# Kernel optimization log

Hardware: AMD Instinct MI355X
Metric: run time of the kernel (lower is better)

## Reference

```python
import jax, jax.numpy as jnp
import numpy as np
from jax import lax

NSAMPLE = 16
NEG_SLOPE = 0.1


def leaky(x):
    return jnp.where(x >= 0, x, NEG_SLOPE * x)


def setup_inputs() -> dict:
    key = jax.random.key(0)
    ks = jax.random.split(key, 8)
    B, N1, N2, D = 4, 4096, 4096, 64
    C_in, C_mid, C_out = D + D + 3, 128, 128  # 131 -> 128 -> 128
    xyz1 = jax.random.normal(ks[0], (B, 3, N1), jnp.float32)
    xyz2 = jax.random.normal(ks[1], (B, 3, N2), jnp.float32)
    points1 = jax.random.normal(ks[2], (B, D, N1), jnp.float32)
    points2 = jax.random.normal(ks[3], (B, D, N2), jnp.float32)
    W1 = jax.random.normal(ks[4], (C_mid, C_in), jnp.float32) * 0.05
    b1 = jnp.zeros((C_mid,), jnp.float32)
    W2 = jax.random.normal(ks[5], (C_out, C_mid), jnp.float32) * 0.05
    b2 = jnp.zeros((C_out,), jnp.float32)
    return {"xyz1": xyz1, "xyz2": xyz2, "points1": points1, "points2": points2,
            "W1": W1, "b1": b1, "W2": W2, "b2": b2}


def reference(xyz1, xyz2, points1, points2, W1, b1, W2, b2):
    B, _, N1 = xyz1.shape
    x1 = jnp.transpose(xyz1, (0, 2, 1))      # [B,N1,3]
    x2 = jnp.transpose(xyz2, (0, 2, 1))      # [B,N2,3]
    p1 = jnp.transpose(points1, (0, 2, 1))   # [B,N1,D1]
    p2 = jnp.transpose(points2, (0, 2, 1))   # [B,N2,D2]

    # knn_point: k smallest squared distances from each x1 point into x2
    d2 = (jnp.sum(x1 * x1, -1)[:, :, None]
          + jnp.sum(x2 * x2, -1)[:, None, :]
          - 2.0 * jnp.einsum('bnc,bmc->bnm', x1, x2))  # [B,N1,N2]
    _, knn_idx = lax.top_k(-d2, NSAMPLE)     # [B,N1,K]

    bidx = jnp.arange(B)[:, None, None]
    neighbor_xyz = x2[bidx, knn_idx]         # [B,N1,K,3]
    direction_xyz = neighbor_xyz - x1[:, :, None, :]
    gp2 = p2[bidx, knn_idx]                  # [B,N1,K,D2]
    gp1 = jnp.broadcast_to(p1[:, :, None, :], (B, N1, NSAMPLE, p1.shape[-1]))
    feat = jnp.concatenate([gp1, gp2, direction_xyz], axis=-1)  # [B,N1,K,131]

    h = leaky(jnp.einsum('oc,bnkc->bnko', W1, feat) + b1)
    h = leaky(jnp.einsum('oc,bnkc->bnko', W2, h) + b2)           # [B,N1,K,C_out]

    dist = jnp.maximum(jnp.linalg.norm(direction_xyz, axis=3), 1e-10)  # [B,N1,K]
    inv = 1.0 / dist
    weights = inv / jnp.sum(inv, axis=2, keepdims=True)          # [B,N1,K]

    cost = jnp.einsum('bnk,bnko->bon', weights, h)               # [B,C_out,N1]
    return cost
```

## Files before the change

### kernel.cpp

```cpp
#include <hip/hip_runtime.h>

typedef unsigned short u16;
typedef unsigned int u32;
typedef unsigned long long u64;
typedef __bf16 bf16x8 __attribute__((ext_vector_type(8)));
typedef float f32x4 __attribute__((ext_vector_type(4)));

#define MFMA16(a, b, c) __builtin_amdgcn_mfma_f32_16x16x32_bf16(a, b, c, 0, 0, 0)

static __device__ __forceinline__ u16 f2bf(float f) {
  union { float f; u32 u; } v; v.f = f;
  u32 u = v.u;
  u32 r = (u + 0x7FFFu + ((u >> 16) & 1u)) >> 16;
  return (u16)r;
}

static __device__ __forceinline__ bf16x8 ld16(const u16* p) {
  return __builtin_bit_cast(bf16x8, *(const uint4*)p);
}

static __device__ __forceinline__ u64 u64min(u64 a, u64 b) { return a < b ? a : b; }

static __device__ __forceinline__ u64 bitonic64(u64 v, int lane) {
#pragma unroll
  for (int k = 2; k <= 64; k <<= 1) {
#pragma unroll
    for (int j = k >> 1; j > 0; j >>= 1) {
      u64 o = __shfl_xor(v, j, 64);
      bool up = ((lane & k) == 0);
      bool lower = ((lane & j) == 0);
      u64 mn = v < o ? v : o;
      u64 mx = v < o ? o : v;
      v = (lower == up) ? mn : mx;
    }
  }
  return v;
}

static __device__ __forceinline__ void bitonic64_2(u64& a, u64& b, int lane) {
#pragma unroll
  for (int k = 2; k <= 64; k <<= 1) {
#pragma unroll
    for (int j = k >> 1; j > 0; j >>= 1) {
      u64 oa = __shfl_xor(a, j, 64);
      u64 ob = __shfl_xor(b, j, 64);
      bool up = ((lane & k) == 0);
      bool lower = ((lane & j) == 0);
      bool sel = (lower == up);
      u64 mna = a < oa ? a : oa, mxa = a < oa ? oa : a;
      u64 mnb = b < ob ? b : ob, mxb = b < ob ? ob : b;
      a = sel ? mna : mxa;
      b = sel ? mnb : mxb;
    }
  }
}

static __device__ __forceinline__ void bitonic32_2(u64& a, u64& b, int lane) {
#pragma unroll
  for (int k = 2; k <= 32; k <<= 1) {
#pragma unroll
    for (int j = k >> 1; j > 0; j >>= 1) {
      u64 oa = __shfl_xor(a, j, 64);
      u64 ob = __shfl_xor(b, j, 64);
      bool up = ((lane & k) == 0);
      bool lower = ((lane & j) == 0);
      bool sel = (lower == up);
      u64 mna = a < oa ? a : oa, mxa = a < oa ? oa : a;
      u64 mnb = b < ob ? b : ob, mxb = b < ob ? ob : b;
      a = sel ? mna : mxa;
      b = sel ? mnb : mxb;
    }
  }
}

static __device__ __forceinline__ u32 fkey(float f) {
  u32 bb = __float_as_uint(f);
  u32 sgn = (u32)((int)bb >> 31);
  return bb ^ (sgn | 0x80000000u);
}

static __device__ __forceinline__ float ikey(u32 k) {
  u32 bb = (k & 0x80000000u) ? (k ^ 0x80000000u) : ~k;
  return __uint_as_float(bb);
}

static __device__ __forceinline__ float d2of(float x, float y, float z, float s1,
                                             f32x4 c) {
  float dt = __builtin_fmaf(z, c[2], __builtin_fmaf(y, c[1], __fmul_rn(x, c[0])));
  return __fsub_rn(__fadd_rn(s1, c[3]), __fmul_rn(2.0f, dt));
}

__global__ __launch_bounds__(1024, 2) void knn_prep(
    const float* __restrict__ xyz1, const float* __restrict__ xyz2,
    const float* __restrict__ points1, const float* __restrict__ points2,
    const float* __restrict__ W1, const float* __restrict__ W2,
    u16* __restrict__ p1t, u16* __restrict__ p2t,
    u16* __restrict__ W1b, u16* __restrict__ W2b,
    int* __restrict__ knn) {
  __shared__ __align__(16) char LB[65536];
  f32x4* candL = (f32x4*)LB;
  u16* tile = (u16*)LB;
  __shared__ u64 surv[16][2][64];
  const int t = threadIdx.x;
  const int lane = t & 63;
  const int w = t >> 6;
  const int g = blockIdx.x;

  if (g < 36) {
    int i = g * 1024 + t;
    if (i < 128 * 160) {
      int r = i / 160, c = i - r * 160;
      W1b[i] = (c < 131) ? f2bf(W1[r * 131 + c]) : (u16)0;
    } else {
      int u = i - 128 * 160;
      W2b[u] = f2bf(W2[u]);
    }
  }

  {
    const float* src = (g < 256) ? points1 : points2;
    u16* dst = (g < 256) ? p1t : p2t;
    const int gb = g & 255;
    const int tb = gb >> 6;
    const int n0 = (gb & 63) << 6;
    const float* sp = src + ((size_t)tb << 18);
#pragma unroll
    for (int i = 0; i < 4; i++) {
      int d = (i << 4) + (t >> 6);
      int n = t & 63;
      tile[n * 66 + d] = f2bf(sp[((size_t)d << 12) + n0 + n]);
    }
    __syncthreads();
    u16* dp = dst + ((size_t)(tb * 4096 + n0) << 6);
#pragma unroll
    for (int i = 0; i < 2; i++) {
      int n = (i << 5) + (t >> 5);
      int dp2 = t & 31;
      *(u32*)(dp + n * 64 + (dp2 << 1)) = *(const u32*)(tile + n * 66 + (dp2 << 1));
    }
  }
  __syncthreads();

  const int b = g >> 7;
  const int rbase = (g & 127) << 5;
  const float* X1 = xyz1 + b * 12288;
  const float* X2 = xyz2 + b * 12288;
#pragma unroll
  for (int i = 0; i < 4; i++) {
    int m = i * 1024 + t;
    float x = X2[m], y = X2[4096 + m], z = X2[8192 + m];
    float s2 = __fadd_rn(__fadd_rn(__fmul_rn(x, x), __fmul_rn(y, y)),
                         __fmul_rn(z, z));
    f32x4 pk = {x, y, z, s2};
    candL[m] = pk;
  }
  __syncthreads();

  {
    const int n0 = rbase + (w << 1);
    const int n1 = n0 + 1;
    const int row0 = b * 4096 + n0;
    const int row1 = row0 + 1;
    const float x0 = X1[n0], y0 = X1[4096 + n0], z0 = X1[8192 + n0];
    const float x1 = X1[n1], y1 = X1[4096 + n1], z1 = X1[8192 + n1];
    const float s10 = __fadd_rn(__fadd_rn(__fmul_rn(x0, x0), __fmul_rn(y0, y0)),
                                __fmul_rn(z0, z0));
    const float s11 = __fadd_rn(__fadd_rn(__fmul_rn(x1, x1), __fmul_rn(y1, y1)),
                                __fmul_rn(z1, z1));

    float fm0 = 3e38f, fm1 = 3e38f;
#pragma unroll 8
    for (int j = 0; j < 64; j++) {
      f32x4 c = candL[(j << 6) + lane];
      fm0 = fminf(fm0, d2of(x0, y0, z0, s10, c));
      fm1 = fminf(fm1, d2of(x1, y1, z1, s11, c));
    }

    const u32 k0 = fkey(fm0), k1 = fkey(fm1);
    u32 lo0 = 0u, hi0 = 0xFFFFFFFFu, lo1 = 0u, hi1 = 0xFFFFFFFFu;
#pragma unroll
    for (int it = 0; it < 32; it++) {
      u32 md0 = lo0 + ((hi0 - lo0) >> 1);
      u32 md1 = lo1 + ((hi1 - lo1) >> 1);
      bool ge0 = __popcll(__ballot(k0 <= md0)) >= 16;
      bool ge1 = __popcll(__ballot(k1 <= md1)) >= 16;
      hi0 = ge0 ? md0 : hi0;  lo0 = ge0 ? lo0 : md0 + 1;
      hi1 = ge1 ? md1 : hi1;  lo1 = ge1 ? lo1 : md1 + 1;
    }
    const float tau0 = ikey(hi0);
    const float tau1 = ikey(hi1);

    u32 base0 = 0, base1 = 0;
#pragma unroll 8
    for (int j = 0; j < 64; j++) {
      const int m = (j << 6) + lane;
      f32x4 c = candL[m];
      float d0 = d2of(x0, y0, z0, s10, c);
      float d1 = d2of(x1, y1, z1, s11, c);
      bool p0 = d0 <= tau0;
      bool p1 = d1 <= tau1;
      u64 mk0 = __ballot(p0);
      u64 mk1 = __ballot(p1);
      if (mk0) {
        if (p0) {
          u32 pre = __builtin_amdgcn_mbcnt_lo((u32)mk0, 0u);
          pre = __builtin_amdgcn_mbcnt_hi((u32)(mk0 >> 32), pre);
          u32 slot = base0 + pre;
          if (slot < 64u) surv[w][0][slot] = ((u64)fkey(d0) << 32) | (u32)m;
        }
        base0 += (u32)__popcll(mk0);
      }
      if (mk1) {
        if (p1) {
          u32 pre = __builtin_amdgcn_mbcnt_lo((u32)mk1, 0u);
          pre = __builtin_amdgcn_mbcnt_hi((u32)(mk1 >> 32), pre);
          u32 slot = base1 + pre;
          if (slot < 64u) surv[w][1][slot] = ((u64)fkey(d1) << 32) | (u32)m;
        }
        base1 += (u32)__popcll(mk1);
      }
    }
    const u32 S0 = base0, S1 = base1;

    const u32 Smax = max(S0, S1);
    if (Smax <= 32) {
      u64 v0 = (lane < (int)S0) ? surv[w][0][lane] : ~0ull;
      u64 v1 = (lane < (int)S1) ? surv[w][1][lane] : ~0ull;
      bitonic32_2(v0, v1, lane);
      if (lane < 16) {
        knn[row0 * 16 + lane] = (int)(v0 & 0xFFFFFFFFull);
        knn[row1 * 16 + lane] = (int)(v1 & 0xFFFFFFFFull);
      }
    } else if (Smax <= 64) {
      u64 v0 = (lane < (int)S0) ? surv[w][0][lane] : ~0ull;
      u64 v1 = (lane < (int)S1) ? surv[w][1][lane] : ~0ull;
      bitonic64_2(v0, v1, lane);
      if (lane < 16) {
        knn[row0 * 16 + lane] = (int)(v0 & 0xFFFFFFFFull);
        knn[row1 * 16 + lane] = (int)(v1 & 0xFFFFFFFFull);
      }
    } else {
#pragma unroll 1
      for (int p = 0; p < 2; p++) {
        const u32 S = p ? S1 : S0;
        const int row = p ? row1 : row0;
        const float xx = p ? x1 : x0, yy = p ? y1 : y0, zz = p ? z1 : z0;
        const float ss = p ? s11 : s10;
        if (S <= 64) {
          u64 v = (lane < (int)S) ? surv[w][p][lane] : ~0ull;
          v = bitonic64(v, lane);
          if (lane < 16) knn[row * 16 + lane] = (int)(v & 0xFFFFFFFFull);
        } else {
          u64 prev = 0;
          for (int rr = 0; rr < 16; rr++) {
            u64 lm = ~0ull;
#pragma unroll 8
            for (int j = 0; j < 64; j++) {
              const int m = (j << 6) + lane;
              f32x4 c = candL[m];
              float d = d2of(xx, yy, zz, ss, c);
              u64 k64 = ((u64)fkey(d) << 32) | (u32)m;
              if (k64 > prev && k64 < lm) lm = k64;
            }
            u64 gm = lm;
#pragma unroll
            for (int off = 32; off; off >>= 1)
              gm = u64min(gm, __shfl_xor(gm, off, 64));
            if (lane == 0) knn[row * 16 + rr] = (int)(gm & 0xFFFFFFFFull);
            prev = gm;
          }
        }
      }
    }
  }
}

__global__ __launch_bounds__(256, 3) void mlp_kernel(
    const float* __restrict__ xyz1, const float* __restrict__ xyz2,
    const u16* __restrict__ p1t, const u16* __restrict__ p2t,
    const int* __restrict__ knn,
    const u16* __restrict__ W1b, const float* __restrict__ b1,
    const u16* __restrict__ W2b, const float* __restrict__ b2,
    float* __restrict__ out) {
  __shared__ __align__(16) u16 F[128 * 168];
  __shared__ __align__(16) float winv[128];
  __shared__ __align__(16) float wnorm[128];
  __shared__ __align__(16) float outbuf[128 * 12];
  const int t = threadIdx.x;
  const int g = blockIdx.x;
  const int b = g >> 9;
  const int rbase = (g & 511) << 3;

  {
    const int m = t >> 1, half = t & 1;
    const int n1 = rbase + (m >> 4);
    const uint4* s1p = (const uint4*)(p1t + ((size_t)(b * 4096 + n1) << 6)) + half * 4;
    uint4* d1p = (uint4*)(F + m * 168) + half * 4;
    d1p[0] = s1p[0]; d1p[1] = s1p[1]; d1p[2] = s1p[2]; d1p[3] = s1p[3];
    const int idx = knn[(((size_t)(b * 4096 + n1)) << 4) + (m & 15)];
    const uint4* s2p = (const uint4*)(p2t + ((size_t)(b * 4096 + idx) << 6)) + half * 4;
    uint4* d2p = (uint4*)(F + m * 168 + 64) + half * 4;
    d2p[0] = s2p[0]; d2p[1] = s2p[1]; d2p[2] = s2p[2]; d2p[3] = s2p[3];
  }
  if (t < 128) {
    const int m = t;
    const int n1 = rbase + (m >> 4);
    const int idx = knn[(((size_t)(b * 4096 + n1)) << 4) + (m & 15)];
    const float* X1 = xyz1 + b * 12288;
    const float* X2 = xyz2 + b * 12288;
    float dx = X2[idx] - X1[n1];
    float dy = X2[4096 + idx] - X1[4096 + n1];
    float dz = X2[8192 + idx] - X1[8192 + n1];
    u32 u0 = (u32)f2bf(dx) | ((u32)f2bf(dy) << 16);
    u32 u1 = (u32)f2bf(dz);
    uint4 pk = make_uint4(u0, u1, 0u, 0u);
    *(uint4*)(F + m * 168 + 128) = pk;
    float d = sqrtf(dx * dx + dy * dy + dz * dz);
    winv[m] = 1.0f / fmaxf(d, 1e-10f);
  } else {
    const int m = t - 128;
    uint4 zz = make_uint4(0u, 0u, 0u, 0u);
    uint4* zp = (uint4*)(F + m * 168 + 136);
    zp[0] = zz; zp[1] = zz; zp[2] = zz; zp[3] = zz;
  }
  __syncthreads();

  if (t < 128) {
    const int r = t >> 4;
    float s = 0.f;
#pragma unroll
    for (int k = 0; k < 16; k++) s += winv[(r << 4) + k];
    wnorm[t] = winv[t] / s;
  }

  const int lane = t & 63;
  const int wid = t >> 6;
  const int l15 = lane & 15;
  const int quad = lane >> 4;
  const int koff = quad << 3;
  const int nbase = wid << 5;

  f32x4 acc[8][2];
  const f32x4 z4 = {0.f, 0.f, 0.f, 0.f};
#pragma unroll
  for (int i = 0; i < 8; i++)
#pragma unroll
    for (int j = 0; j < 2; j++) acc[i][j] = z4;

#pragma unroll
  for (int s = 0; s < 5; s++) {
    bf16x8 bf0 = ld16(W1b + (nbase + l15) * 160 + s * 32 + koff);
    bf16x8 bf1 = ld16(W1b + (nbase + 16 + l15) * 160 + s * 32 + koff);
#pragma unroll
    for (int mt = 0; mt < 8; mt++) {
      bf16x8 a = ld16(F + (mt * 16 + l15) * 168 + s * 32 + koff);
      acc[mt][0] = MFMA16(a, bf0, acc[mt][0]);
      acc[mt][1] = MFMA16(a, bf1, acc[mt][1]);
    }
  }
  __syncthreads();

  {
    const float bv0 = b1[nbase + l15];
    const float bv1 = b1[nbase + 16 + l15];
#pragma unroll
    for (int mt = 0; mt < 8; mt++) {
      u16* hrow = F + (mt * 16 + quad * 4) * 168;
#pragma unroll
      for (int r = 0; r < 4; r++) {
        float zv0 = acc[mt][0][r] + bv0;
        zv0 = (zv0 >= 0.f) ? zv0 : 0.1f * zv0;
        hrow[r * 168 + nbase + l15] = f2bf(zv0);
        float zv1 = acc[mt][1][r] + bv1;
        zv1 = (zv1 >= 0.f) ? zv1 : 0.1f * zv1;
        hrow[r * 168 + nbase + 16 + l15] = f2bf(zv1);
      }
    }
  }
  __syncthreads();

  f32x4 acc2[8][2];
#pragma unroll
  for (int i = 0; i < 8; i++)
#pragma unroll
    for (int j = 0; j < 2; j++) acc2[i][j] = z4;

#pragma unroll
  for (int s = 0; s < 4; s++) {
    bf16x8 bf0 = ld16(W2b + (nbase + l15) * 128 + s * 32 + koff);
    bf16x8 bf1 = ld16(W2b + (nbase + 16 + l15) * 128 + s * 32 + koff);
#pragma unroll
    for (int mt = 0; mt < 8; mt++) {
      bf16x8 a = ld16(F + (mt * 16 + l15) * 168 + s * 32 + koff);
      acc2[mt][0] = MFMA16(a, bf0, acc2[mt][0]);
      acc2[mt][1] = MFMA16(a, bf1, acc2[mt][1]);
    }
  }

  {
    const float bv0 = b2[nbase + l15];
    const float bv1 = b2[nbase + 16 + l15];
#pragma unroll
    for (int mt = 0; mt < 8; mt++) {
      const f32x4 w4 = *(const f32x4*)&wnorm[(mt << 4) + (quad << 2)];
      float p0 = 0.f, p1 = 0.f;
#pragma unroll
      for (int r = 0; r < 4; r++) {
        float zv0 = acc2[mt][0][r] + bv0;
        zv0 = (zv0 >= 0.f) ? zv0 : 0.1f * zv0;
        p0 += zv0 * w4[r];
        float zv1 = acc2[mt][1][r] + bv1;
        zv1 = (zv1 >= 0.f) ? zv1 : 0.1f * zv1;
        p1 += zv1 * w4[r];
      }
      p0 += __shfl_xor(p0, 16); p0 += __shfl_xor(p0, 32);
      p1 += __shfl_xor(p1, 16); p1 += __shfl_xor(p1, 32);
      if (quad == 0) {
        outbuf[(nbase + l15) * 12 + mt] = p0;
        outbuf[(nbase + 16 + l15) * 12 + mt] = p1;
      }
    }
  }
  __syncthreads();
  {
    const int ch = t >> 1, half = t & 1;
    f32x4 v = *(const f32x4*)&outbuf[ch * 12 + (half << 2)];
    float* op = out + (((size_t)(b * 128 + ch)) << 12) + rbase + (half << 2);
    *(f32x4*)op = v;
  }
}

extern "C" void kernel_launch(void* const* d_in, const int* in_sizes, int n_in,
                              void* d_out, int out_size, void* d_ws, size_t ws_size,
                              hipStream_t stream) {
  const float* xyz1 = (const float*)d_in[0];
  const float* xyz2 = (const float*)d_in[1];
  const float* points1 = (const float*)d_in[2];
  const float* points2 = (const float*)d_in[3];
  const float* W1 = (const float*)d_in[4];
  const float* b1 = (const float*)d_in[5];
  const float* W2 = (const float*)d_in[6];
  const float* b2 = (const float*)d_in[7];
  float* out = (float*)d_out;

  char* ws = (char*)d_ws;
  int* knn = (int*)ws;
  u16* p1t = (u16*)(ws + 1048576);
  u16* p2t = (u16*)(ws + 3145728);
  u16* W1b = (u16*)(ws + 5242880);
  u16* W2b = (u16*)(ws + 5283840);

  hipLaunchKernelGGL(knn_prep, dim3(512), dim3(1024), 0, stream,
                     xyz1, xyz2, points1, points2, W1, W2, p1t, p2t, W1b, W2b, knn);
  hipLaunchKernelGGL(mlp_kernel, dim3(2048), dim3(256), 0, stream,
                     xyz1, xyz2, p1t, p2t, knn, W1b, b1, W2b, b2, out);
}
```

Before: 143.6 us.

## Shrink knn_prep blocks and read candidates from global instead of LDS

```diff
diff --git a/kernel.cpp b/kernel.cpp
--- a/kernel.cpp
+++ b/kernel.cpp
@@ -90,24 +90,31 @@
   return __fsub_rn(__fadd_rn(s1, c[3]), __fmul_rn(2.0f, dt));
 }
 
-__global__ __launch_bounds__(1024, 2) void knn_prep(
+static __device__ __forceinline__ f32x4 candOf(const float* X2, int m) {
+  float cx = X2[m], cy = X2[4096 + m], cz = X2[8192 + m];
+  float cs = __fadd_rn(__fadd_rn(__fmul_rn(cx, cx), __fmul_rn(cy, cy)),
+                       __fmul_rn(cz, cz));
+  f32x4 c = {cx, cy, cz, cs};
+  return c;
+}
+
+__global__ __launch_bounds__(256, 7) void knn_prep(
     const float* __restrict__ xyz1, const float* __restrict__ xyz2,
     const float* __restrict__ points1, const float* __restrict__ points2,
     const float* __restrict__ W1, const float* __restrict__ W2,
     u16* __restrict__ p1t, u16* __restrict__ p2t,
     u16* __restrict__ W1b, u16* __restrict__ W2b,
     int* __restrict__ knn) {
-  __shared__ __align__(16) char LB[65536];
-  f32x4* candL = (f32x4*)LB;
+  __shared__ __align__(16) char LB[8448];
   u16* tile = (u16*)LB;
-  __shared__ u64 surv[16][2][64];
+  u64 (*surv)[2][64] = (u64(*)[2][64])LB;
   const int t = threadIdx.x;
   const int lane = t & 63;
   const int w = t >> 6;
   const int g = blockIdx.x;
 
-  if (g < 36) {
-    int i = g * 1024 + t;
+  if (g < 144) {
+    int i = g * 256 + t;
     if (i < 128 * 160) {
       int r = i / 160, c = i - r * 160;
       W1b[i] = (c < 131) ? f2bf(W1[r * 131 + c]) : (u16)0;
@@ -118,44 +125,39 @@
   }
 
   {
+    const bool doT = (g < 512);
     const float* src = (g < 256) ? points1 : points2;
     u16* dst = (g < 256) ? p1t : p2t;
     const int gb = g & 255;
     const int tb = gb >> 6;
     const int n0 = (gb & 63) << 6;
     const float* sp = src + ((size_t)tb << 18);
-#pragma unroll
-    for (int i = 0; i < 4; i++) {
-      int d = (i << 4) + (t >> 6);
-      int n = t & 63;
-      tile[n * 66 + d] = f2bf(sp[((size_t)d << 12) + n0 + n]);
+    if (doT) {
+#pragma unroll
+      for (int i = 0; i < 16; i++) {
+        int d = (i << 2) + (t >> 6);
+        int n = t & 63;
+        tile[n * 66 + d] = f2bf(sp[((size_t)d << 12) + n0 + n]);
+      }
     }
     __syncthreads();
-    u16* dp = dst + ((size_t)(tb * 4096 + n0) << 6);
-#pragma unroll
-    for (int i = 0; i < 2; i++) {
-      int n = (i << 5) + (t >> 5);
-      int dp2 = t & 31;
-      *(u32*)(dp + n * 64 + (dp2 << 1)) = *(const u32*)(tile + n * 66 + (dp2 << 1));
+    if (doT) {
+      u16* dp = dst + ((size_t)(tb * 4096 + n0) << 6);
+#pragma unroll
+      for (int i = 0; i < 8; i++) {
+        int n = (i << 3) + (t >> 5);
+        int dp2 = t & 31;
+        *(u32*)(dp + n * 64 + (dp2 << 1)) =
+            *(const u32*)(tile + n * 66 + (dp2 << 1));
+      }
     }
   }
   __syncthreads();
 
-  const int b = g >> 7;
-  const int rbase = (g & 127) << 5;
+  const int b = g >> 9;
+  const int rbase = (g & 511) << 3;
   const float* X1 = xyz1 + b * 12288;
   const float* X2 = xyz2 + b * 12288;
-#pragma unroll
-  for (int i = 0; i < 4; i++) {
-    int m = i * 1024 + t;
-    float x = X2[m], y = X2[4096 + m], z = X2[8192 + m];
-    float s2 = __fadd_rn(__fadd_rn(__fmul_rn(x, x), __fmul_rn(y, y)),
-                         __fmul_rn(z, z));
-    f32x4 pk = {x, y, z, s2};
-    candL[m] = pk;
-  }
-  __syncthreads();
-
   {
     const int n0 = rbase + (w << 1);
     const int n1 = n0 + 1;
@@ -169,9 +171,9 @@
                                 __fmul_rn(z1, z1));
 
     float fm0 = 3e38f, fm1 = 3e38f;
-#pragma unroll 8
+#pragma unroll 4
     for (int j = 0; j < 64; j++) {
-      f32x4 c = candL[(j << 6) + lane];
+      f32x4 c = candOf(X2, (j << 6) + lane);
       fm0 = fminf(fm0, d2of(x0, y0, z0, s10, c));
       fm1 = fminf(fm1, d2of(x1, y1, z1, s11, c));
     }
@@ -191,10 +193,10 @@
     const float tau1 = ikey(hi1);
 
     u32 base0 = 0, base1 = 0;
-#pragma unroll 8
+#pragma unroll 4
     for (int j = 0; j < 64; j++) {
       const int m = (j << 6) + lane;
-      f32x4 c = candL[m];
+      f32x4 c = candOf(X2, m);
       float d0 = d2of(x0, y0, z0, s10, c);
       float d1 = d2of(x1, y1, z1, s11, c);
       bool p0 = d0 <= tau0;
@@ -254,10 +256,10 @@
           u64 prev = 0;
           for (int rr = 0; rr < 16; rr++) {
             u64 lm = ~0ull;
-#pragma unroll 8
+#pragma unroll 4
             for (int j = 0; j < 64; j++) {
               const int m = (j << 6) + lane;
-              f32x4 c = candL[m];
+              f32x4 c = candOf(X2, m);
               float d = d2of(xx, yy, zz, ss, c);
               u64 k64 = ((u64)fkey(d) << 32) | (u32)m;
               if (k64 > prev && k64 < lm) lm = k64;
@@ -450,7 +452,7 @@
   u16* W1b = (u16*)(ws + 5242880);
   u16* W2b = (u16*)(ws + 5283840);
 
-  hipLaunchKernelGGL(knn_prep, dim3(512), dim3(1024), 0, stream,
+  hipLaunchKernelGGL(knn_prep, dim3(2048), dim3(256), 0, stream,
                      xyz1, xyz2, points1, points2, W1, W2, p1t, p2t, W1b, W2b, knn);
   hipLaunchKernelGGL(mlp_kernel, dim3(2048), dim3(256), 0, stream,
                      xyz1, xyz2, p1t, p2t, knn, W1b, b1, W2b, b2, out);
```

After: 149.2 us. 3.9% more time.
